# Kernel tuning notes

Hardware: AMD Instinct MI355X
Metric: run time of the kernel (lower is better)

## Reference

```python
import jax, jax.numpy as jnp
import numpy as np

N_NODES = 50000
N_GRAPHS = 64
IN_DIM, HIDDEN, OUT_DIM = 2063, 256, 128
E_L, E_G = 800000, 1600000


def setup_inputs() -> dict:
    key = jax.random.key(0)
    ks = jax.random.split(key, 16)
    x = jax.random.normal(ks[0], (N_NODES, IN_DIM), dtype=jnp.float32)
    edge_index_l = jax.random.randint(ks[1], (2, E_L), 0, N_NODES, dtype=jnp.int64)
    edge_index_g = jax.random.randint(ks[2], (2, E_G), 0, N_NODES, dtype=jnp.int64)
    batch = jnp.sort(jax.random.randint(ks[3], (N_NODES,), 0, N_GRAPHS, dtype=jnp.int64))

    def glorot(k, shape):
        scale = jnp.sqrt(2.0 / (shape[0] + shape[1])).astype(jnp.float32)
        return jax.random.normal(k, shape, dtype=jnp.float32) * scale

    return {
        "x": x,
        "edge_index_l": edge_index_l,
        "edge_index_g": edge_index_g,
        "batch": batch,
        "W_l1": glorot(ks[4], (IN_DIM, HIDDEN)), "b_l1": jnp.zeros((HIDDEN,), jnp.float32),
        "W_l2": glorot(ks[5], (HIDDEN, OUT_DIM)), "b_l2": jnp.zeros((OUT_DIM,), jnp.float32),
        "W_g1": glorot(ks[6], (IN_DIM, HIDDEN)), "b_g1": jnp.zeros((HIDDEN,), jnp.float32),
        "W_g2": glorot(ks[7], (HIDDEN, OUT_DIM)), "b_g2": jnp.zeros((OUT_DIM,), jnp.float32),
        "W_fuse": glorot(ks[8], (2 * OUT_DIM, OUT_DIM)), "b_fuse": jnp.zeros((OUT_DIM,), jnp.float32),
    }


def gcn_conv(x, edge_index, W, b):
    # PyG GCNConv: add self loops, symmetric D^{-1/2}(A+I)D^{-1/2} normalization,
    # linear transform then scatter-add aggregation at target nodes.
    n = x.shape[0]
    loops = jnp.arange(n, dtype=edge_index.dtype)
    src = jnp.concatenate([edge_index[0], loops])
    dst = jnp.concatenate([edge_index[1], loops])
    deg = jax.ops.segment_sum(jnp.ones_like(dst, dtype=x.dtype), dst, num_segments=n)
    dinv = jax.lax.rsqrt(deg)  # deg >= 1 due to self loops
    norm = dinv[src] * dinv[dst]  # [E+n]
    h = x @ W  # [n, out]
    msg = h[src] * norm[:, None]  # gather + scale
    return jax.ops.segment_sum(msg, dst, num_segments=n) + b


def global_mean_pool(x, batch, num_graphs):
    sums = jax.ops.segment_sum(x, batch, num_segments=num_graphs)
    cnt = jax.ops.segment_sum(jnp.ones((x.shape[0],), x.dtype), batch, num_segments=num_graphs)
    return sums / jnp.maximum(cnt, 1.0)[:, None]


def reference(x, edge_index_l, edge_index_g, batch,
              W_l1, b_l1, W_l2, b_l2, W_g1, b_g1, W_g2, b_g2, W_fuse, b_fuse):
    # dropout is identity in eval mode
    xl = jax.nn.relu(gcn_conv(x, edge_index_l, W_l1, b_l1))
    xl = gcn_conv(xl, edge_index_l, W_l2, b_l2)
    xl = global_mean_pool(xl, batch, N_GRAPHS)

    xg = jax.nn.relu(gcn_conv(x, edge_index_g, W_g1, b_g1))
    xg = gcn_conv(xg, edge_index_g, W_g2, b_g2)
    xg = global_mean_pool(xg, batch, N_GRAPHS)

    out = jnp.concatenate([xl, xg], axis=1)  # [G, 2*out_dim]
    return jax.nn.relu(out @ W_fuse + b_fuse)
```

## Files before the change

kernel.cpp:

```cpp
#include <hip/hip_runtime.h>
#include <hip/hip_bf16.h>
#include <cstdint>
#include <cstddef>


#define N_NODES 50000
#define N_GRAPHS 64
#define IN_DIM 2063
#define HIDDEN 256
#define OUT_DIM 128
#define EDGES_L 800000
#define EDGES_G 1600000
#define HCOLS 512
#define KPAD 2112
#define MPAD 50048
#define GBM 64
#define NGB (MPAD / GBM)
#define NT (KPAD / 32)
#define PCH 256
#define NCHUNK ((N_NODES + PCH - 1) / PCH)

#define QUARTER 12544
#define SL_L 64
#define SL_G 128
#define EPS 12500
#define HBLOCKS (4 * (SL_L + SL_G))

typedef __attribute__((ext_vector_type(8))) __bf16 bf16x8;
typedef __attribute__((ext_vector_type(4))) float f32x4;

__device__ __forceinline__ float bf2f(unsigned short u) {
  union { unsigned int i; float f; } c; c.i = ((unsigned int)u) << 16; return c.f;
}
__device__ __forceinline__ unsigned short f2bf(float f) {
  __hip_bfloat16 h = __float2bfloat16(f);
  return *reinterpret_cast<unsigned short*>(&h);
}
__device__ __forceinline__ unsigned char f2fp8(float f) {
  return (unsigned char)(__builtin_amdgcn_cvt_pk_fp8_f32(f, f, 0, 0) & 0xff);
}

__global__ void k_cvt_w(const float* __restrict__ Wl, const float* __restrict__ Wg,
                        unsigned short* __restrict__ Wt) {
  int i = blockIdx.x * blockDim.x + threadIdx.x;
  if (i >= HCOLS * KPAD) return;
  int n = i / KPAD;
  int k = i - n * KPAD;
  float v = 0.f;
  if (k < IN_DIM) {
    v = (n < HIDDEN) ? Wl[(size_t)k * HIDDEN + n] : Wg[(size_t)k * HIDDEN + (n - HIDDEN)];
  }
  Wt[(size_t)n * KPAD + k] = f2bf(v);
}

__launch_bounds__(256)
__global__ void k_hist(const int* __restrict__ dstL, const int* __restrict__ dstG,
                       int* __restrict__ partL, int* __restrict__ partG) {
  __shared__ int hist[QUARTER];
  const int i = blockIdx.x;
  const int* __restrict__ dst;
  int slice, q;
  int* __restrict__ part;
  if (i < 4 * SL_L) {
    slice = i >> 2; q = i & 3;
    dst = dstL;
    part = partL + (size_t)(slice * 4 + q) * QUARTER;
  } else {
    int j = i - 4 * SL_L;
    slice = j >> 2; q = j & 3;
    dst = dstG;
    part = partG + (size_t)(slice * 4 + q) * QUARTER;
  }
  for (int t = threadIdx.x; t < QUARTER; t += 256) hist[t] = 0;
  __syncthreads();
  const int e0 = slice * EPS;
  const int qbase = q * QUARTER;
  for (int e = e0 + threadIdx.x; e < e0 + EPS; e += 256) {
    int d = dst[e] - qbase;
    if ((unsigned)d < QUARTER) atomicAdd(&hist[d], 1);
  }
  __syncthreads();
  for (int t = threadIdx.x; t < QUARTER; t += 256) part[t] = hist[t];
}

__global__ void k_prefix(int* __restrict__ partL, int* __restrict__ partG,
                         const int* __restrict__ batch, int* __restrict__ degL,
                         int* __restrict__ degG, float* __restrict__ dinvL,
                         float* __restrict__ dinvG, float* __restrict__ cL,
                         float* __restrict__ cG) {
  int t = blockIdx.x * blockDim.x + threadIdx.x;
  if (t >= 8 * QUARTER) return;
  const int b = t / (4 * QUARTER);
  const int n = t - b * 4 * QUARTER;
  const int q = n / QUARTER, loc = n - q * QUARTER;
  const int NS = b ? SL_G : SL_L;
  int* p = (b ? partG : partL) + (size_t)q * QUARTER + loc;
  int run = 0;
  for (int s = 0; s < NS; s++) {
    int* pp = p + (size_t)s * 4 * QUARTER;
    int v = *pp;
    *pp = run;
    run += v;
  }
  if (n < N_NODES) {
    float d = 1.0f / sqrtf((float)(run + 1));
    if (b == 0) {
      degL[n] = run; dinvL[n] = d; cL[(size_t)n * 64 + batch[n]] = d * d;
    } else {
      degG[n] = run; dinvG[n] = d; cG[(size_t)n * 64 + batch[n]] = d * d;
    }
  }
}

__global__ void k_scan1(const int* __restrict__ degL, const int* __restrict__ degG,
                        int* __restrict__ rowL, int* __restrict__ rowG,
                        const int* __restrict__ batch, int* __restrict__ start) {
  if (blockIdx.x >= 2) {
    int n = (blockIdx.x - 2) * 1024 + threadIdx.x;
    if (n >= N_NODES) return;
    int bn = batch[n];
    int bp = n ? batch[n - 1] : -1;
    for (int g = bp + 1; g <= bn; g++) start[g] = n;
    if (n == N_NODES - 1)
      for (int g = bn + 1; g <= N_GRAPHS; g++) start[g] = N_NODES;
    return;
  }
  __shared__ int part[1024];
  const int t = threadIdx.x;
  const int* __restrict__ deg = blockIdx.x ? degG : degL;
  int* __restrict__ row = blockIdx.x ? rowG : rowL;
  const int c0 = t * 49;
  int s = 0;
  for (int j = 0; j < 49; j++) {
    int idx = c0 + j;
    s += (idx < N_NODES) ? deg[idx] : 0;
  }
  part[t] = s;
  __syncthreads();
  for (int ofs = 1; ofs < 1024; ofs <<= 1) {
    int v = (t >= ofs) ? part[t - ofs] : 0;
    __syncthreads();
    part[t] += v;
    __syncthreads();
  }
  int run = (t > 0) ? part[t - 1] : 0;
  for (int j = 0; j < 49; j++) {
    int idx = c0 + j;
    if (idx < N_NODES) { row[idx] = run; run += deg[idx]; }
  }
  if (t == 1023) row[N_NODES] = part[1023];
}

__launch_bounds__(256)
__global__ void k_gemm_scat(const float* __restrict__ X,
                            const unsigned short* __restrict__ Wt,
                            unsigned char* __restrict__ H,
                            const int* __restrict__ srcL, const int* __restrict__ dstL,
                            const int* __restrict__ srcG, const int* __restrict__ dstG,
                            const int* __restrict__ partL, const int* __restrict__ partG,
                            const int* __restrict__ rowL, const int* __restrict__ rowG,
                            const float* __restrict__ dinvL, const float* __restrict__ dinvG,
                            const int* __restrict__ batch, int2* __restrict__ erL,
                            int2* __restrict__ erG, float* __restrict__ cL,
                            float* __restrict__ cG) {
  __shared__ __align__(16) char lds[2 * 4096 + 2 * 32768];

  if (blockIdx.x >= NGB) {
    int* hist = (int*)lds;
    const int i = blockIdx.x - NGB;
    const int *src, *dst, *part, *row;
    const float* dinv;
    int2* er;
    float* c;
    int slice, q;
    if (i < 4 * SL_L) {
      slice = i >> 2; q = i & 3;
      src = srcL; dst = dstL; row = rowL; dinv = dinvL; er = erL; c = cL;
      part = partL + (size_t)(slice * 4 + q) * QUARTER;
    } else {
      int j = i - 4 * SL_L;
      slice = j >> 2; q = j & 3;
      src = srcG; dst = dstG; row = rowG; dinv = dinvG; er = erG; c = cG;
      part = partG + (size_t)(slice * 4 + q) * QUARTER;
    }
    for (int t = threadIdx.x; t < QUARTER; t += 256) hist[t] = 0;
    __syncthreads();
    const int e0 = slice * EPS;
    const int qbase = q * QUARTER;
    for (int e = e0 + threadIdx.x; e < e0 + EPS; e += 256) {
      int d = dst[e];
      int loc = d - qbase;
      if ((unsigned)loc < QUARTER) {
        int s = src[e];
        int rank = atomicAdd(&hist[loc], 1);
        int pos = row[d] + part[loc] + rank;
        float nrm = dinv[s] * dinv[d];
        er[pos] = make_int2(s, __float_as_int(nrm));
        atomicAdd(&c[(size_t)s * 64 + batch[d]], nrm);
      }
    }
    return;
  }

  char* const Ab0 = lds;
  char* const Ab1 = lds + 4096;
  char* const Bb0 = lds + 8192;
  char* const Bb1 = lds + 8192 + 32768;
  const int tid = threadIdx.x;
  const int lane = tid & 63;
  const int wave = tid >> 6;
  const int brow = blockIdx.x * GBM;

  const int ar = tid >> 2;
  const int ach = tid & 3;
  const int askew = (ar >> 1) & 3;
  const int asrc = (ach ^ askew) * 8;
  const int arow_g = brow + ar;
  const bool aok = arow_g < N_NODES;
  const float* __restrict__ Arow = X + (size_t)arow_g * IN_DIM;

  const int fr = lane & 15;
  const int fq = lane >> 4;

  f32x4 acc[4][8];
  const f32x4 zero = {0.f, 0.f, 0.f, 0.f};
#pragma unroll
  for (int m = 0; m < 4; m++)
#pragma unroll
    for (int n = 0; n < 8; n++) acc[m][n] = zero;

#pragma unroll
  for (int i = 0; i < 8; i++) {
    const int s = i * 256 + tid;
    const int row = s >> 2, cch = s & 3;
    const unsigned short* g = Wt + (size_t)row * KPAD + ((cch ^ ((row >> 1) & 3)) * 8);
    __builtin_amdgcn_global_load_lds(
        (const __attribute__((address_space(1))) void*)g,
        (__attribute__((address_space(3))) void*)(Bb0 + (i * 256 + wave * 64) * 16),
        16, 0, 0);
  }
  float a[8];
#pragma unroll
  for (int j = 0; j < 8; j++) a[j] = aok ? Arow[asrc + j] : 0.f;
  {
    uint u0 = (uint)f2bf(a[0]) | ((uint)f2bf(a[1]) << 16);
    uint u1 = (uint)f2bf(a[2]) | ((uint)f2bf(a[3]) << 16);
    uint u2 = (uint)f2bf(a[4]) | ((uint)f2bf(a[5]) << 16);
    uint u3 = (uint)f2bf(a[6]) | ((uint)f2bf(a[7]) << 16);
    *(uint4*)(Ab0 + tid * 16) = make_uint4(u0, u1, u2, u3);
  }
  __syncthreads();

  for (int t = 0; t < NT; ++t) {
    const int k0 = t * 32;
    char* const Acur = (t & 1) ? Ab1 : Ab0;
    char* const Bcur = (t & 1) ? Bb1 : Bb0;
    char* const Anxt = (t & 1) ? Ab0 : Ab1;
    char* const Bnxt = (t & 1) ? Bb0 : Bb1;

    if (t + 1 < NT) {
      const int kn = k0 + 32;
#pragma unroll
      for (int i = 0; i < 8; i++) {
        const int s = i * 256 + tid;
        const int row = s >> 2, cch = s & 3;
        const unsigned short* g = Wt + (size_t)row * KPAD + kn + ((cch ^ ((row >> 1) & 3)) * 8);
        __builtin_amdgcn_global_load_lds(
            (const __attribute__((address_space(1))) void*)g,
            (__attribute__((address_space(3))) void*)(Bnxt + (i * 256 + wave * 64) * 16),
            16, 0, 0);
      }
      const int kb = kn + asrc;
      if (aok) {
        if (kb + 7 < IN_DIM) {
#pragma unroll
          for (int j = 0; j < 8; j++) a[j] = Arow[kb + j];
        } else {
#pragma unroll
          for (int j = 0; j < 8; j++) a[j] = (kb + j < IN_DIM) ? Arow[kb + j] : 0.f;
        }
      }
    }

    {
      __builtin_amdgcn_s_setprio(1);
      bf16x8 bv[8];
#pragma unroll
      for (int n = 0; n < 8; n++) {
        const int row = wave * 128 + n * 16 + fr;
        bv[n] = *(const bf16x8*)(Bcur + row * 64 + ((fq ^ ((row >> 1) & 3)) * 16));
      }
#pragma unroll
      for (int m = 0; m < 4; m++) {
        const int row = m * 16 + fr;
        bf16x8 av = *(const bf16x8*)(Acur + row * 64 + ((fq ^ ((row >> 1) & 3)) * 16));
#pragma unroll
        for (int n = 0; n < 8; n++)
          acc[m][n] = __builtin_amdgcn_mfma_f32_16x16x32_bf16(av, bv[n], acc[m][n], 0, 0, 0);
      }
      __builtin_amdgcn_s_setprio(0);
    }

    if (t + 1 < NT) {
      uint u0 = (uint)f2bf(a[0]) | ((uint)f2bf(a[1]) << 16);
      uint u1 = (uint)f2bf(a[2]) | ((uint)f2bf(a[3]) << 16);
      uint u2 = (uint)f2bf(a[4]) | ((uint)f2bf(a[5]) << 16);
      uint u3 = (uint)f2bf(a[6]) | ((uint)f2bf(a[7]) << 16);
      *(uint4*)(Anxt + tid * 16) = make_uint4(u0, u1, u2, u3);
    }
    __syncthreads();
  }

#pragma unroll
  for (int m = 0; m < 4; m++) {
    const int r0 = brow + m * 16 + fq * 4;
#pragma unroll
    for (int n = 0; n < 8; n++) {
      const int col = wave * 128 + n * 16 + fr;
#pragma unroll
      for (int j = 0; j < 4; j++) {
        int r = r0 + j;
        if (r < N_NODES) H[(size_t)r * HCOLS + col] = f2fp8(acc[m][n][j]);
      }
    }
  }
}

__global__ void k_agg(const unsigned char* __restrict__ h,
                      const float* __restrict__ dinvL, const float* __restrict__ dinvG,
                      const int* __restrict__ rowL, const int* __restrict__ rowG,
                      const int2* __restrict__ erL, const int2* __restrict__ erG,
                      const float* __restrict__ biasL, const float* __restrict__ biasG,
                      unsigned short* __restrict__ xl) {
  const int br = blockIdx.y;
  const int node = blockIdx.x * 4 + (threadIdx.x >> 6);
  const int lane = threadIdx.x & 63;
  const float* __restrict__ dinv = br ? dinvG : dinvL;
  const int* __restrict__ rp = br ? rowG : rowL;
  const int2* __restrict__ er = br ? erG : erL;
  const float* __restrict__ bias = br ? biasG : biasL;
  const int off = br ? 256 : 0;
  const size_t lcol = off + lane * 4;

  float di = dinv[node];
  float w0 = di * di;
  uint u = *(const uint*)(h + (size_t)node * HCOLS + lcol);
  float a0 = w0 * __builtin_amdgcn_cvt_f32_fp8(u, 0);
  float a1 = w0 * __builtin_amdgcn_cvt_f32_fp8(u, 1);
  float a2 = w0 * __builtin_amdgcn_cvt_f32_fp8(u, 2);
  float a3 = w0 * __builtin_amdgcn_cvt_f32_fp8(u, 3);

  int e = rp[node];
  const int e1 = rp[node + 1];
  for (; e + 16 <= e1; e += 16) {
    int2 r[16];
    uint v[16];
#pragma unroll
    for (int j = 0; j < 16; j++) r[j] = er[e + j];
#pragma unroll
    for (int j = 0; j < 16; j++)
      v[j] = *(const uint*)(h + (size_t)r[j].x * HCOLS + lcol);
#pragma unroll
    for (int j = 0; j < 16; j++) {
      float w = __int_as_float(r[j].y);
      a0 = fmaf(w, __builtin_amdgcn_cvt_f32_fp8(v[j], 0), a0);
      a1 = fmaf(w, __builtin_amdgcn_cvt_f32_fp8(v[j], 1), a1);
      a2 = fmaf(w, __builtin_amdgcn_cvt_f32_fp8(v[j], 2), a2);
      a3 = fmaf(w, __builtin_amdgcn_cvt_f32_fp8(v[j], 3), a3);
    }
  }
  for (; e + 4 <= e1; e += 4) {
    int2 r[4];
    uint v[4];
#pragma unroll
    for (int j = 0; j < 4; j++) r[j] = er[e + j];
#pragma unroll
    for (int j = 0; j < 4; j++)
      v[j] = *(const uint*)(h + (size_t)r[j].x * HCOLS + lcol);
#pragma unroll
    for (int j = 0; j < 4; j++) {
      float w = __int_as_float(r[j].y);
      a0 = fmaf(w, __builtin_amdgcn_cvt_f32_fp8(v[j], 0), a0);
      a1 = fmaf(w, __builtin_amdgcn_cvt_f32_fp8(v[j], 1), a1);
      a2 = fmaf(w, __builtin_amdgcn_cvt_f32_fp8(v[j], 2), a2);
      a3 = fmaf(w, __builtin_amdgcn_cvt_f32_fp8(v[j], 3), a3);
    }
  }
  for (; e < e1; e++) {
    int2 r = er[e];
    float w = __int_as_float(r.y);
    uint v = *(const uint*)(h + (size_t)r.x * HCOLS + lcol);
    a0 = fmaf(w, __builtin_amdgcn_cvt_f32_fp8(v, 0), a0);
    a1 = fmaf(w, __builtin_amdgcn_cvt_f32_fp8(v, 1), a1);
    a2 = fmaf(w, __builtin_amdgcn_cvt_f32_fp8(v, 2), a2);
    a3 = fmaf(w, __builtin_amdgcn_cvt_f32_fp8(v, 3), a3);
  }
  float4 b = *(const float4*)(bias + lane * 4);
  ushort4 o;
  o.x = f2bf(fmaxf(a0 + b.x, 0.f));
  o.y = f2bf(fmaxf(a1 + b.y, 0.f));
  o.z = f2bf(fmaxf(a2 + b.z, 0.f));
  o.w = f2bf(fmaxf(a3 + b.w, 0.f));
  *(ushort4*)(xl + (size_t)node * HCOLS + lcol) = o;
}

__launch_bounds__(256)
__global__ void k_pool2(const unsigned short* __restrict__ xl,
                        const float* __restrict__ cL, const float* __restrict__ cG,
                        float* __restrict__ Spart) {
  __shared__ float cs[64][64];
  const int t = threadIdx.x;
  const int chunk = blockIdx.x;
  const int br = blockIdx.y;
  const float* __restrict__ C = br ? cG : cL;
  const int xoff = br ? 256 : 0;
  const int n0 = chunk * PCH;
  float acc[64];
#pragma unroll
  for (int g = 0; g < 64; g++) acc[g] = 0.f;

  for (int tile = 0; tile < PCH; tile += 64) {
    const int base = n0 + tile;
    __syncthreads();
#pragma unroll
    for (int i = 0; i < 16; i++) {
      int idx = i * 256 + t;
      int nn = idx >> 6, gg = idx & 63;
      int node = base + nn;
      cs[nn][gg] = (node < N_NODES) ? C[(size_t)node * 64 + gg] : 0.f;
    }
    __syncthreads();
    for (int nn = 0; nn < 64; nn++) {
      int node = base + nn;
      float v = (node < N_NODES) ? bf2f(xl[(size_t)node * HCOLS + xoff + t]) : 0.f;
#pragma unroll
      for (int g4 = 0; g4 < 16; g4++) {
        float4 cv = *(const float4*)&cs[nn][g4 * 4];
        acc[g4 * 4 + 0] = fmaf(cv.x, v, acc[g4 * 4 + 0]);
        acc[g4 * 4 + 1] = fmaf(cv.y, v, acc[g4 * 4 + 1]);
        acc[g4 * 4 + 2] = fmaf(cv.z, v, acc[g4 * 4 + 2]);
        acc[g4 * 4 + 3] = fmaf(cv.w, v, acc[g4 * 4 + 3]);
      }
    }
  }
  float* sp = Spart + ((size_t)br * NCHUNK + chunk) * 16384 + t;
#pragma unroll
  for (int g = 0; g < 64; g++) sp[g * 256] = acc[g];
}

__global__ void k_pool_reduce(const float* __restrict__ Spart, float* __restrict__ S) {
  int i = blockIdx.x * blockDim.x + threadIdx.x;
  if (i >= 2 * 16384) return;
  int br = i >> 14, idx = i & 16383;
  const float* p = Spart + (size_t)br * NCHUNK * 16384 + idx;
  float s = 0.f;
  for (int ch = 0; ch < NCHUNK; ch++) s += p[(size_t)ch * 16384];
  S[i] = s;
}

__global__ void k_final(const float* __restrict__ S,
                        const float* __restrict__ Wl2, const float* __restrict__ bl2,
                        const float* __restrict__ Wg2, const float* __restrict__ bg2,
                        const float* __restrict__ Wf, const float* __restrict__ bf,
                        const int* __restrict__ start, float* __restrict__ out) {
  __shared__ float pl[OUT_DIM], pg[OUT_DIM];
  int g = blockIdx.x, t = threadIdx.x;
  float invc = 1.0f / fmaxf((float)(start[g + 1] - start[g]), 1.0f);
  const float* Sl = S + (size_t)g * HIDDEN;
  const float* Sg = S + (size_t)N_GRAPHS * HIDDEN + (size_t)g * HIDDEN;
  float al = 0.f, ag = 0.f;
  for (int k = 0; k < HIDDEN; k++) {
    al = fmaf(Sl[k], Wl2[k * OUT_DIM + t], al);
    ag = fmaf(Sg[k], Wg2[k * OUT_DIM + t], ag);
  }
  pl[t] = al * invc + bl2[t];
  pg[t] = ag * invc + bg2[t];
  __syncthreads();
  float o = bf[t];
  for (int j = 0; j < OUT_DIM; j++) {
    o = fmaf(pl[j], Wf[j * OUT_DIM + t], o);
    o = fmaf(pg[j], Wf[(OUT_DIM + j) * OUT_DIM + t], o);
  }
  out[(size_t)g * OUT_DIM + t] = fmaxf(o, 0.f);
}

extern "C" void kernel_launch(void* const* d_in, const int* in_sizes, int n_in,
                              void* d_out, int out_size, void* d_ws, size_t ws_size,
                              hipStream_t stream) {
  const float* x = (const float*)d_in[0];
  const int* el = (const int*)d_in[1];
  const int* eg = (const int*)d_in[2];
  const int* batch = (const int*)d_in[3];
  const float* Wl1 = (const float*)d_in[4];
  const float* bl1 = (const float*)d_in[5];
  const float* Wl2 = (const float*)d_in[6];
  const float* bl2 = (const float*)d_in[7];
  const float* Wg1 = (const float*)d_in[8];
  const float* bg1 = (const float*)d_in[9];
  const float* Wg2 = (const float*)d_in[10];
  const float* bg2 = (const float*)d_in[11];
  const float* Wf = (const float*)d_in[12];
  const float* bf = (const float*)d_in[13];
  float* out = (float*)d_out;
  char* ws = (char*)d_ws;

  const size_t NPAD = 200192;
  size_t off = 0;
  float* c_l = (float*)(ws + off); off += (size_t)N_NODES * 64 * 4;
  float* c_g = (float*)(ws + off); off += (size_t)N_NODES * 64 * 4;
  const size_t zero_bytes = off;
  int* start = (int*)(ws + off); off += 512;
  float* S = (float*)(ws + off); off += (size_t)2 * N_GRAPHS * HIDDEN * 4;
  int* deg_l = (int*)(ws + off); off += NPAD;
  int* deg_g = (int*)(ws + off); off += NPAD;
  float* dinv_l = (float*)(ws + off); off += NPAD;
  float* dinv_g = (float*)(ws + off); off += NPAD;
  int* row_l = (int*)(ws + off); off += NPAD;
  int* row_g = (int*)(ws + off); off += NPAD;
  int* partL = (int*)(ws + off); off += (size_t)SL_L * 4 * QUARTER * 4;
  int* partG = (int*)(ws + off); off += (size_t)SL_G * 4 * QUARTER * 4;
  int2* er_l = (int2*)(ws + off); off += (size_t)EDGES_L * 8;
  int2* er_g = (int2*)(ws + off); off += (size_t)EDGES_G * 8;
  unsigned short* Wt = (unsigned short*)(ws + off); off += (size_t)HCOLS * KPAD * 2;
  unsigned char* h = (unsigned char*)(ws + off); off += (size_t)N_NODES * HCOLS;
  unsigned short* xl = (unsigned short*)(ws + off); off += (size_t)N_NODES * HCOLS * 2;
  float* Spart = (float*)partL;

  const int* srcL = el;
  const int* dstL = el + EDGES_L;
  const int* srcG = eg;
  const int* dstG = eg + EDGES_G;

  hipMemsetAsync(ws, 0, zero_bytes, stream);

  k_cvt_w<<<(HCOLS * KPAD + 255) / 256, 256, 0, stream>>>(Wl1, Wg1, Wt);

  k_hist<<<HBLOCKS, 256, 0, stream>>>(dstL, dstG, partL, partG);
  k_prefix<<<(8 * QUARTER + 255) / 256, 256, 0, stream>>>(partL, partG, batch, deg_l, deg_g,
                                                          dinv_l, dinv_g, c_l, c_g);
  k_scan1<<<51, 1024, 0, stream>>>(deg_l, deg_g, row_l, row_g, batch, start);

  k_gemm_scat<<<NGB + HBLOCKS, 256, 0, stream>>>(x, Wt, h, srcL, dstL, srcG, dstG,
                                                 partL, partG, row_l, row_g, dinv_l, dinv_g,
                                                 batch, er_l, er_g, c_l, c_g);

  dim3 agrid(N_NODES / 4, 2);
  k_agg<<<agrid, 256, 0, stream>>>(h, dinv_l, dinv_g, row_l, row_g, er_l, er_g, bl1, bg1, xl);

  dim3 pgrid(NCHUNK, 2);
  k_pool2<<<pgrid, 256, 0, stream>>>(xl, c_l, c_g, Spart);
  k_pool_reduce<<<(2 * 16384 + 255) / 256, 256, 0, stream>>>(Spart, S);

  k_final<<<N_GRAPHS, OUT_DIM, 0, stream>>>(S, Wl2, bl2, Wg2, bg2, Wf, bf, start, out);
}
```

Measured before the change: 862.1 us.

## Move pooling-coefficient atomics from GEMM-scatter kernel into aggregation kernel

Moves the per-edge atomicAdd that builds the pooling coefficient matrices c_L/c_G out of the scatter blocks co-running with the GEMM. They now run in extra blocks appended to the aggregation launch, which becomes a 1D grid with the branch derived from the block index. The aim is to shorten the scatter blocks so they hide behind the GEMM, and to overlap the scattered atomics with the gather-bound aggregation. The extra blocks are scheduled after the aggregation blocks, so they may extend the tail of that kernel.

```diff
diff --git a/kernel.cpp b/kernel.cpp
--- a/kernel.cpp
+++ b/kernel.cpp
@@ -19,6 +19,7 @@
 #define NT (KPAD / 32)
 #define PCH 256
 #define NCHUNK ((N_NODES + PCH - 1) / PCH)
+#define NAGGB (N_NODES / 4)
 
 #define QUARTER 12544
 #define SL_L 64
@@ -160,9 +161,7 @@
                             const int* __restrict__ partL, const int* __restrict__ partG,
                             const int* __restrict__ rowL, const int* __restrict__ rowG,
                             const float* __restrict__ dinvL, const float* __restrict__ dinvG,
-                            const int* __restrict__ batch, int2* __restrict__ erL,
-                            int2* __restrict__ erG, float* __restrict__ cL,
-                            float* __restrict__ cG) {
+                            int2* __restrict__ erL, int2* __restrict__ erG) {
   __shared__ __align__(16) char lds[2 * 4096 + 2 * 32768];
 
   if (blockIdx.x >= NGB) {
@@ -171,16 +170,15 @@
     const int *src, *dst, *part, *row;
     const float* dinv;
     int2* er;
-    float* c;
     int slice, q;
     if (i < 4 * SL_L) {
       slice = i >> 2; q = i & 3;
-      src = srcL; dst = dstL; row = rowL; dinv = dinvL; er = erL; c = cL;
+      src = srcL; dst = dstL; row = rowL; dinv = dinvL; er = erL;
       part = partL + (size_t)(slice * 4 + q) * QUARTER;
     } else {
       int j = i - 4 * SL_L;
       slice = j >> 2; q = j & 3;
-      src = srcG; dst = dstG; row = rowG; dinv = dinvG; er = erG; c = cG;
+      src = srcG; dst = dstG; row = rowG; dinv = dinvG; er = erG;
       part = partG + (size_t)(slice * 4 + q) * QUARTER;
     }
     for (int t = threadIdx.x; t < QUARTER; t += 256) hist[t] = 0;
@@ -194,9 +192,7 @@
         int s = src[e];
         int rank = atomicAdd(&hist[loc], 1);
         int pos = row[d] + part[loc] + rank;
-        float nrm = dinv[s] * dinv[d];
-        er[pos] = make_int2(s, __float_as_int(nrm));
-        atomicAdd(&c[(size_t)s * 64 + batch[d]], nrm);
+        er[pos] = make_int2(s, __float_as_int(dinv[s] * dinv[d]));
       }
     }
     return;
@@ -331,9 +327,30 @@
                       const int* __restrict__ rowL, const int* __restrict__ rowG,
                       const int2* __restrict__ erL, const int2* __restrict__ erG,
                       const float* __restrict__ biasL, const float* __restrict__ biasG,
-                      unsigned short* __restrict__ xl) {
-  const int br = blockIdx.y;
-  const int node = blockIdx.x * 4 + (threadIdx.x >> 6);
+                      unsigned short* __restrict__ xl,
+                      const int* __restrict__ srcL, const int* __restrict__ dstL,
+                      const int* __restrict__ srcG, const int* __restrict__ dstG,
+                      const int* __restrict__ batch, float* __restrict__ cL,
+                      float* __restrict__ cG) {
+  const int b = blockIdx.x;
+  if (b >= 2 * NAGGB) {
+    const int tot = EDGES_L + EDGES_G;
+    for (int e = (b - 2 * NAGGB) * 256 + threadIdx.x; e < tot; e += HBLOCKS * 256) {
+      if (e < EDGES_L) {
+        int s = srcL[e], d = dstL[e];
+        atomicAdd(&cL[(size_t)s * 64 + batch[d]], dinvL[s] * dinvL[d]);
+      } else {
+        int ee = e - EDGES_L;
+        int s = srcG[ee], d = dstG[ee];
+        atomicAdd(&cG[(size_t)s * 64 + batch[d]], dinvG[s] * dinvG[d]);
+      }
+    }
+    return;
+  }
+
+  const int br = (b >= NAGGB) ? 1 : 0;
+  const int bx = br ? (b - NAGGB) : b;
+  const int node = bx * 4 + (threadIdx.x >> 6);
   const int lane = threadIdx.x & 63;
   const float* __restrict__ dinv = br ? dinvG : dinvL;
   const int* __restrict__ rp = br ? rowG : rowL;
@@ -395,12 +412,12 @@
     a2 = fmaf(w, __builtin_amdgcn_cvt_f32_fp8(v, 2), a2);
     a3 = fmaf(w, __builtin_amdgcn_cvt_f32_fp8(v, 3), a3);
   }
-  float4 b = *(const float4*)(bias + lane * 4);
+  float4 bb = *(const float4*)(bias + lane * 4);
   ushort4 o;
-  o.x = f2bf(fmaxf(a0 + b.x, 0.f));
-  o.y = f2bf(fmaxf(a1 + b.y, 0.f));
-  o.z = f2bf(fmaxf(a2 + b.z, 0.f));
-  o.w = f2bf(fmaxf(a3 + b.w, 0.f));
+  o.x = f2bf(fmaxf(a0 + bb.x, 0.f));
+  o.y = f2bf(fmaxf(a1 + bb.y, 0.f));
+  o.z = f2bf(fmaxf(a2 + bb.z, 0.f));
+  o.w = f2bf(fmaxf(a3 + bb.w, 0.f));
   *(ushort4*)(xl + (size_t)node * HCOLS + lcol) = o;
 }
 
@@ -542,10 +559,11 @@
 
   k_gemm_scat<<<NGB + HBLOCKS, 256, 0, stream>>>(x, Wt, h, srcL, dstL, srcG, dstG,
                                                  partL, partG, row_l, row_g, dinv_l, dinv_g,
-                                                 batch, er_l, er_g, c_l, c_g);
-
-  dim3 agrid(N_NODES / 4, 2);
-  k_agg<<<agrid, 256, 0, stream>>>(h, dinv_l, dinv_g, row_l, row_g, er_l, er_g, bl1, bg1, xl);
+                                                 er_l, er_g);
+
+  k_agg<<<2 * NAGGB + HBLOCKS, 256, 0, stream>>>(h, dinv_l, dinv_g, row_l, row_g,
+                                                 er_l, er_g, bl1, bg1, xl,
+                                                 srcL, dstL, srcG, dstG, batch, c_l, c_g);
 
   dim3 pgrid(NCHUNK, 2);
   k_pool2<<<pgrid, 256, 0, stream>>>(xl, c_l, c_g, Spart);
```

New measurement: 914.6 us. 6.1% more time.
